# Kernel optimization log

Measured on AMD Instinct MI355X. Metric: run time of the kernel, lower is better.

Reference implementation:

```python
import jax, jax.numpy as jnp
import numpy as np
import math

D_MODEL = 1024
D_STATE = 16
D_CONV = 4
EXPAND = 2
D_INNER = EXPAND * D_MODEL
DT_RANK = math.ceil(D_MODEL / 16)
EPS = 1e-5


def setup_inputs() -> dict:
    key = jax.random.key(0)
    ks = jax.random.split(key, 8)
    B, L = 2, 1024
    s = 0.02
    return {
        "hidden_states": jax.random.normal(ks[0], (B, L, D_MODEL), jnp.float32),
        "norm_weight": jnp.ones((D_MODEL,), jnp.float32),
        "in_proj_w": (jax.random.normal(ks[1], (2 * D_INNER, D_MODEL), jnp.float32) * s),
        "conv_w": (jax.random.normal(ks[2], (D_INNER, D_CONV), jnp.float32) * s),
        "conv_b": jnp.zeros((D_INNER,), jnp.float32),
        "x_proj_w": (jax.random.normal(ks[3], (DT_RANK + 2 * D_STATE, D_INNER), jnp.float32) * s),
        "dt_proj_w": (jax.random.normal(ks[4], (D_INNER, DT_RANK), jnp.float32) * s),
        "dt_proj_b": jax.random.uniform(ks[5], (D_INNER,), jnp.float32, -4.0, -2.0),
        "A_log": jnp.log(jnp.broadcast_to(jnp.arange(1, D_STATE + 1, dtype=jnp.float32), (D_INNER, D_STATE))),
        "D": jnp.ones((D_INNER,), jnp.float32),
        "out_proj_w": (jax.random.normal(ks[6], (D_MODEL, D_INNER), jnp.float32) * s),
    }


def _rmsnorm(x, w):
    # Faithful to source: rms = ||x||_2 / sqrt(d); x / (rms + eps) * w
    norm = jnp.linalg.norm(x, axis=-1, keepdims=True)
    rms = norm * (1.0 / math.sqrt(x.shape[-1]))
    return w * (x / (rms + EPS))


def _mamba(h, in_proj_w, conv_w, conv_b, x_proj_w, dt_proj_w, dt_proj_b, A_log, D, out_proj_w):
    B, L, _ = h.shape
    xz = h @ in_proj_w.T                      # (B,L,2*D_INNER)
    x, z = jnp.split(xz, 2, axis=-1)          # each (B,L,D_INNER)

    # causal depthwise conv1d along L, kernel D_CONV
    xpad = jnp.pad(x, ((0, 0), (D_CONV - 1, 0), (0, 0)))
    xc = conv_b
    for k in range(D_CONV):                   # tiny fixed loop over kernel taps
        xc = xc + xpad[:, k:k + L, :] * conv_w[:, k]
    xc = jax.nn.silu(xc)                      # (B,L,D_INNER)

    x_dbl = xc @ x_proj_w.T                   # (B,L,DT_RANK+2N)
    dt, Bm, Cm = jnp.split(x_dbl, [DT_RANK, DT_RANK + D_STATE], axis=-1)
    dt = jax.nn.softplus(dt @ dt_proj_w.T + dt_proj_b)   # (B,L,D_INNER)

    A = -jnp.exp(A_log)                       # (D_INNER,N)
    deltaA = jnp.exp(dt[..., None] * A)                      # (B,L,D_INNER,N)
    deltaBu = (dt * xc)[..., None] * Bm[:, :, None, :]        # (B,L,D_INNER,N)

    def step(hst, inp):
        dA, dBu, Ct = inp
        hst = dA * hst + dBu                  # (B,D_INNER,N)
        y = jnp.einsum('bdn,bn->bd', hst, Ct)
        return hst, y

    h0 = jnp.zeros((B, D_INNER, D_STATE), xc.dtype)
    _, ys = jax.lax.scan(step, h0, (deltaA.swapaxes(0, 1), deltaBu.swapaxes(0, 1), Cm.swapaxes(0, 1)))
    y = ys.swapaxes(0, 1)                     # (B,L,D_INNER)
    y = y + D * xc
    y = y * jax.nn.silu(z)
    return y @ out_proj_w.T                   # (B,L,D_MODEL)


def reference(hidden_states, norm_weight, in_proj_w, conv_w, conv_b, x_proj_w,
              dt_proj_w, dt_proj_b, A_log, D, out_proj_w):
    residual = hidden_states
    h = _rmsnorm(residual, norm_weight)
    out = _mamba(h, in_proj_w, conv_w, conv_b, x_proj_w, dt_proj_w, dt_proj_b,
                 A_log, D, out_proj_w)
    return out, residual
```

## Files before the change

kernel.cpp:

```cpp
#include <hip/hip_runtime.h>

typedef __bf16 bf16x8 __attribute__((ext_vector_type(8)));
typedef float f32x4 __attribute__((ext_vector_type(4)));

__device__ __forceinline__ float b2f(ushort u) {
    union { unsigned int i; float f; } v;
    v.i = ((unsigned int)u) << 16;
    return v.f;
}
__device__ __forceinline__ ushort f2b(float f) {
    union { float f; unsigned int i; } v;
    v.f = f;
    unsigned int x = v.i;
    unsigned int r = (x + 0x7fffu + ((x >> 16) & 1u)) >> 16;
    return (ushort)r;
}
__device__ __forceinline__ float fexp2(float x) {
#if __has_builtin(__builtin_amdgcn_exp2f)
    return __builtin_amdgcn_exp2f(x);
#else
    return exp2f(x);
#endif
}
__device__ __forceinline__ unsigned int packb2(float ap, float h) {
    return ((unsigned int)f2b(h) << 16) | (unsigned int)f2b(ap);
}
__device__ __forceinline__ void gload16(const ushort* g, ushort* l) {
    __builtin_amdgcn_global_load_lds(
        (const __attribute__((address_space(1))) unsigned int*)g,
        (__attribute__((address_space(3))) unsigned int*)l, 16, 0, 0);
}
__device__ __forceinline__ bf16x8 ldsfrag(const ushort* s, int row, int cq) {
    int p = cq ^ (row & 7);
    return *(const bf16x8*)(s + row * 64 + p * 8);
}

#define D_MODEL 1024
#define D_INNER 2048
#define D_STATE 16
#define DT_RANK 64
#define NTOK    2048
#define LSEQ    1024
#define NCH     64
#define LC      16
#define KSL     16
#define LOG2E   1.44269504088896f

__global__ __launch_bounds__(256) void prep_kernel(
    const float* __restrict__ hs, const float* __restrict__ w,
    ushort* __restrict__ hout, float* __restrict__ resid,
    const float* __restrict__ inproj, const float* __restrict__ outproj,
    const float* __restrict__ xprojw, const float* __restrict__ dtw,
    ushort* __restrict__ wIn, ushort* __restrict__ wOut,
    ushort* __restrict__ xpw, ushort* __restrict__ dtwb,
    float* __restrict__ xdbl)
{
    int blk = blockIdx.x;
    int tid = threadIdx.x;
    if (blk < NTOK) {
        int t = blk;
        float4 r4 = *(const float4*)(hs + (size_t)t * D_MODEL + tid * 4);
        float s = r4.x * r4.x + r4.y * r4.y + r4.z * r4.z + r4.w * r4.w;
        #pragma unroll
        for (int off = 32; off >= 1; off >>= 1) s += __shfl_xor(s, off);
        __shared__ float red[4];
        int lane = tid & 63, wid = tid >> 6;
        if (lane == 0) red[wid] = s;
        __syncthreads();
        float tot = red[0] + red[1] + red[2] + red[3];
        float inv = 1.0f / (sqrtf(tot) * (1.0f / 32.0f) + 1e-5f);
        float4 w4 = *(const float4*)(w + tid * 4);
        ushort4 o;
        o.x = f2b(w4.x * r4.x * inv);
        o.y = f2b(w4.y * r4.y * inv);
        o.z = f2b(w4.z * r4.z * inv);
        o.w = f2b(w4.w * r4.w * inv);
        *(ushort4*)(hout + (size_t)t * D_MODEL + tid * 4) = o;
        *(float4*)(resid + (size_t)t * D_MODEL + tid * 4) = r4;
    } else if (blk < NTOK + 6464) {
        int i = (blk - NTOK) * 256 + tid;
        const float* src; ushort* dst; int off;
        if (i < 1048576)      { src = inproj;  dst = wIn;  off = i; }
        else if (i < 1572864) { src = outproj; dst = wOut; off = i - 1048576; }
        else if (i < 1622016) { src = xprojw;  dst = xpw;  off = i - 1572864; }
        else if (i < 1654784) { src = dtw;     dst = dtwb; off = i - 1622016; }
        else return;
        float4 v = *(const float4*)(src + (size_t)off * 4);
        ushort4 o;
        o.x = f2b(v.x); o.y = f2b(v.y); o.z = f2b(v.z); o.w = f2b(v.w);
        *(ushort4*)(dst + (size_t)off * 4) = o;
    } else {
        int i = (blk - NTOK - 6464) * 256 + tid;
        if (i < 49152)
            *(float4*)(xdbl + (size_t)i * 4) = (float4){0.f, 0.f, 0.f, 0.f};
    }
}

__global__ __launch_bounds__(512) void gemm_xz_kernel(
    const ushort* __restrict__ Ag, const ushort* __restrict__ Wg,
    const float* __restrict__ cw, const float* __restrict__ cb,
    ushort* __restrict__ xcb, ushort* __restrict__ xb,
    ushort* __restrict__ zq, int K)
{
    __shared__ __align__(16) ushort smem[128 * 128];
    __shared__ float cwl[128][4];
    __shared__ float cbl[128];
    ushort* sA = smem;
    ushort* sB = smem + 128 * 64;
    int tid = threadIdx.x;
    int bm = blockIdx.x, bn = blockIdx.y;
    int wid = tid >> 6, lane = tid & 63;
    int wm = (wid >> 1) * 32, wn = (wid & 1) * 64;
    int l16 = lane & 15, q = lane >> 4;
    int colbase = (bn & 15) * 128;

    if (bn < 16 && tid < 128) {
        cwl[tid][0] = cw[(size_t)(colbase + tid) * 4 + 0];
        cwl[tid][1] = cw[(size_t)(colbase + tid) * 4 + 1];
        cwl[tid][2] = cw[(size_t)(colbase + tid) * 4 + 2];
        cwl[tid][3] = cw[(size_t)(colbase + tid) * 4 + 3];
        cbl[tid] = cb[colbase + tid];
    }

    f32x4 acc[2][4];
    #pragma unroll
    for (int i = 0; i < 2; i++)
        #pragma unroll
        for (int j = 0; j < 4; j++)
            acc[i][j] = (f32x4){0.f, 0.f, 0.f, 0.f};

    const ushort* Abase = Ag + (size_t)bm * 128 * K;
    const ushort* Wbase = Wg + (size_t)bn * 128 * K;

    int segr = lane >> 3, segc = lane & 7;
    size_t goff[2]; int sseg[2];
    #pragma unroll
    for (int t = 0; t < 2; t++) {
        int s = wid * 2 + t;
        int r = s * 8 + segr;
        int gc = segc ^ (r & 7);
        sseg[t] = s * 512;
        goff[t] = (size_t)r * K + gc * 8;
    }

    for (int k0 = 0; k0 < K; k0 += 64) {
        __syncthreads();
        #pragma unroll
        for (int t = 0; t < 2; t++) {
            gload16(Abase + goff[t] + k0, sA + sseg[t]);
            gload16(Wbase + goff[t] + k0, sB + sseg[t]);
        }
        __syncthreads();
        #pragma unroll
        for (int ks = 0; ks < 2; ks++) {
            int cq = ks * 4 + q;
            bf16x8 af[2], bfr[4];
            #pragma unroll
            for (int i = 0; i < 2; i++)
                af[i] = ldsfrag(sA, wm + i * 16 + l16, cq);
            #pragma unroll
            for (int j = 0; j < 4; j++)
                bfr[j] = ldsfrag(sB, wn + j * 16 + l16, cq);
            #pragma unroll
            for (int i = 0; i < 2; i++)
                #pragma unroll
                for (int j = 0; j < 4; j++)
                    acc[i][j] = __builtin_amdgcn_mfma_f32_16x16x32_bf16(af[i], bfr[j], acc[i][j], 0, 0, 0);
        }
    }

    __syncthreads();
    #pragma unroll
    for (int i = 0; i < 2; i++)
        #pragma unroll
        for (int j = 0; j < 4; j++) {
            int col = wn + j * 16 + l16;
            int cchunk = col >> 3, cin = col & 7;
            #pragma unroll
            for (int r = 0; r < 4; r++) {
                int row = wm + i * 16 + q * 4 + r;
                smem[row * 128 + ((cchunk ^ (row & 7)) << 3) + cin] =
                    f2b(acc[i][j][r]);
            }
        }
    __syncthreads();
    size_t rowbase = (size_t)bm * 128;

    if (bn >= 16) {
        int cb2 = (bn - 16) * 128;
        #pragma unroll
        for (int it = 0; it < 4; it++) {
            int flat = it * 4096 + tid * 8;
            int row = flat >> 7, cchunk = (flat & 127) >> 3;
            *(uint4*)(zq + (rowbase + row) * D_INNER + cb2 + (cchunk << 3)) =
                *(const uint4*)(smem + row * 128 + ((cchunk ^ (row & 7)) << 3));
        }
        return;
    }

    if (tid < 96) {
        int rr = tid >> 4;
        int row = (rr < 3) ? rr : (125 + rr - 3);
        int chunk = tid & 15;
        *(uint4*)(xb + (size_t)(bm * 6 + rr) * D_INNER + colbase + chunk * 8) =
            *(const uint4*)(smem + row * 128 + ((chunk ^ (row & 7)) << 3));
    }

    for (int idx = tid; idx < 2000; idx += 512) {
        int row = (idx >> 4) + 3;
        int chunk = idx & 15;
        ushort tap[4][8];
        #pragma unroll
        for (int k = 0; k < 4; k++) {
            int rk = row - 3 + k;
            *(uint4*)tap[k] =
                *(const uint4*)(smem + rk * 128 + ((chunk ^ (rk & 7)) << 3));
        }
        ushort o[8];
        #pragma unroll
        for (int j = 0; j < 8; j++) {
            int cl = chunk * 8 + j;
            float acc2 = cbl[cl];
            #pragma unroll
            for (int k = 0; k < 4; k++)
                acc2 += b2f(tap[k][j]) * cwl[cl][k];
            o[j] = f2b(acc2 / (1.f + __expf(-acc2)));
        }
        *(uint4*)(xcb + (rowbase + row) * D_INNER + colbase + chunk * 8) =
            *(const uint4*)o;
    }
}

__global__ __launch_bounds__(256) void conv_fixup_kernel(
    const ushort* __restrict__ xb, const float* __restrict__ cw,
    const float* __restrict__ cb, ushort* __restrict__ xcb)
{
    int bm = blockIdx.x / 3;
    int r  = blockIdx.x % 3;
    int d0 = threadIdx.x * 8;

    ushort tap[4][8];
    bool has[4];
    #pragma unroll
    for (int k = 0; k < 4; k++) {
        int rt = r - 3 + k;
        if (rt < 0 && (bm & 7) == 0) {
            has[k] = false;
        } else {
            has[k] = true;
            int bmm, slot;
            if (rt < 0) { bmm = bm - 1; slot = rt + 6; }
            else        { bmm = bm;     slot = rt; }
            *(uint4*)tap[k] =
                *(const uint4*)(xb + (size_t)(bmm * 6 + slot) * D_INNER + d0);
        }
    }
    ushort o[8];
    #pragma unroll
    for (int j = 0; j < 8; j++) {
        float4 w4 = *(const float4*)(cw + (size_t)(d0 + j) * 4);
        float wk[4] = {w4.x, w4.y, w4.z, w4.w};
        float acc = cb[d0 + j];
        #pragma unroll
        for (int k = 0; k < 4; k++)
            if (has[k]) acc += b2f(tap[k][j]) * wk[k];
        o[j] = f2b(acc / (1.f + __expf(-acc)));
    }
    *(uint4*)(xcb + (size_t)(bm * 128 + r) * D_INNER + d0) = *(const uint4*)o;
}

__global__ __launch_bounds__(256) void gemm64_kernel(
    const ushort* __restrict__ Ag, const ushort* __restrict__ Wg,
    float* __restrict__ Cf, int M, int N, int K)
{
    __shared__ __align__(16) ushort smem[64 * 128];
    ushort* sA = smem;
    ushort* sB = smem + 64 * 64;
    float* fs = (float*)smem;
    int tid = threadIdx.x;
    int bm = blockIdx.x, bn = blockIdx.y;
    int wid = tid >> 6, lane = tid & 63;
    int wm = wid * 16;
    int l16 = lane & 15, q = lane >> 4;

    f32x4 acc[4];
    #pragma unroll
    for (int j = 0; j < 4; j++) acc[j] = (f32x4){0.f, 0.f, 0.f, 0.f};

    const ushort* Abase = Ag + (size_t)bm * 64 * K;
    const ushort* Wbase = Wg + (size_t)bn * 64 * K;

    int segr = lane >> 3, segc = lane & 7;
    size_t goff[2]; int sseg[2];
    #pragma unroll
    for (int t = 0; t < 2; t++) {
        int s = wid * 2 + t;
        int r = s * 8 + segr;
        int gc = segc ^ (r & 7);
        sseg[t] = s * 512;
        goff[t] = (size_t)r * K + gc * 8;
    }

    for (int k0 = 0; k0 < K; k0 += 64) {
        __syncthreads();
        #pragma unroll
        for (int t = 0; t < 2; t++) {
            gload16(Abase + goff[t] + k0, sA + sseg[t]);
            gload16(Wbase + goff[t] + k0, sB + sseg[t]);
        }
        __syncthreads();
        #pragma unroll
        for (int ks = 0; ks < 2; ks++) {
            int cq = ks * 4 + q;
            bf16x8 af = ldsfrag(sA, wm + l16, cq);
            bf16x8 bfr[4];
            #pragma unroll
            for (int j = 0; j < 4; j++)
                bfr[j] = ldsfrag(sB, j * 16 + l16, cq);
            #pragma unroll
            for (int j = 0; j < 4; j++)
                acc[j] = __builtin_amdgcn_mfma_f32_16x16x32_bf16(af, bfr[j], acc[j], 0, 0, 0);
        }
    }

    __syncthreads();
    #pragma unroll
    for (int j = 0; j < 4; j++)
        #pragma unroll
        for (int r = 0; r < 4; r++)
            fs[(wm + q * 4 + r) * 64 + j * 16 + l16] = acc[j][r];
    __syncthreads();
    #pragma unroll
    for (int it = 0; it < 4; it++) {
        int flat = it * 1024 + tid * 4;
        int row = flat >> 6, col = flat & 63;
        *(float4*)(Cf + (size_t)(bm * 64 + row) * N + bn * 64 + col) =
            *(const float4*)(fs + row * 64 + col);
    }
}

__global__ __launch_bounds__(256) void xproj_partial_kernel(
    const ushort* __restrict__ xcb, const ushort* __restrict__ wq,
    float* __restrict__ xdbl)
{
    __shared__ __align__(16) ushort sA[128 * 40];
    __shared__ __align__(16) ushort sB[96 * 40];
    int tid = threadIdx.x;
    int bm = blockIdx.x, sl = blockIdx.y;
    int wid = tid >> 6, lane = tid & 63;
    int wm = wid * 32;
    int l16 = lane & 15, q = lane >> 4;

    f32x4 acc[2][6];
    #pragma unroll
    for (int i = 0; i < 2; i++)
        #pragma unroll
        for (int j = 0; j < 6; j++)
            acc[i][j] = (f32x4){0.f, 0.f, 0.f, 0.f};

    const ushort* Abase = xcb + (size_t)bm * 128 * D_INNER;
    int kbase = sl * (D_INNER / KSL);

    for (int kk = 0; kk < D_INNER / KSL; kk += 32) {
        int k0 = kbase + kk;
        __syncthreads();
        #pragma unroll
        for (int i = tid; i < 512; i += 256) {
            int r = i >> 2, c = (i & 3) << 3;
            *(uint4*)(sA + r * 40 + c) = *(const uint4*)(Abase + (size_t)r * D_INNER + k0 + c);
        }
        for (int i = tid; i < 384; i += 256) {
            int r = i >> 2, c = (i & 3) << 3;
            *(uint4*)(sB + r * 40 + c) = *(const uint4*)(wq + (size_t)r * D_INNER + k0 + c);
        }
        __syncthreads();
        bf16x8 af[2], bfr[6];
        #pragma unroll
        for (int i = 0; i < 2; i++)
            af[i] = *(const bf16x8*)(sA + (wm + i * 16 + l16) * 40 + q * 8);
        #pragma unroll
        for (int j = 0; j < 6; j++)
            bfr[j] = *(const bf16x8*)(sB + (j * 16 + l16) * 40 + q * 8);
        #pragma unroll
        for (int i = 0; i < 2; i++)
            #pragma unroll
            for (int j = 0; j < 6; j++)
                acc[i][j] = __builtin_amdgcn_mfma_f32_16x16x32_bf16(af[i], bfr[j], acc[i][j], 0, 0, 0);
    }

    int row0 = bm * 128 + wm + q * 4;
    #pragma unroll
    for (int i = 0; i < 2; i++)
        #pragma unroll
        for (int j = 0; j < 6; j++)
            #pragma unroll
            for (int r = 0; r < 4; r++)
                atomicAdd(&xdbl[(size_t)(row0 + i * 16 + r) * 96 + j * 16 + l16],
                          acc[i][j][r]);
}

__global__ __launch_bounds__(256) void dt_gemm_kernel(
    const float* __restrict__ xdbl, const ushort* __restrict__ dtwq,
    const float* __restrict__ dtb, ushort* __restrict__ dtout)
{
    __shared__ __align__(16) ushort sA[64 * 72];
    __shared__ __align__(16) ushort sB[64 * 72];
    int tid = threadIdx.x;
    int bm = blockIdx.x, bn = blockIdx.y;
    int wid = tid >> 6, lane = tid & 63;
    int wm = wid * 16;
    int l16 = lane & 15, q = lane >> 4;

    const float* Abase = xdbl + (size_t)bm * 64 * 96;
    const ushort* Bbase = dtwq + (size_t)bn * 64 * DT_RANK;
    #pragma unroll
    for (int i = tid; i < 512; i += 256) {
        int r = i >> 3, c = (i & 7) << 3;
        float4 v0 = *(const float4*)(Abase + (size_t)r * 96 + c);
        float4 v1 = *(const float4*)(Abase + (size_t)r * 96 + c + 4);
        ushort o[8] = {f2b(v0.x), f2b(v0.y), f2b(v0.z), f2b(v0.w),
                       f2b(v1.x), f2b(v1.y), f2b(v1.z), f2b(v1.w)};
        *(uint4*)(sA + r * 72 + c) = *(const uint4*)o;
        *(uint4*)(sB + r * 72 + c) = *(const uint4*)(Bbase + (size_t)r * DT_RANK + c);
    }
    __syncthreads();

    f32x4 acc[4];
    #pragma unroll
    for (int j = 0; j < 4; j++) acc[j] = (f32x4){0.f, 0.f, 0.f, 0.f};

    #pragma unroll
    for (int ks = 0; ks < 2; ks++) {
        bf16x8 af = *(const bf16x8*)(sA + (wm + l16) * 72 + ks * 32 + q * 8);
        bf16x8 bfr[4];
        #pragma unroll
        for (int j = 0; j < 4; j++)
            bfr[j] = *(const bf16x8*)(sB + (j * 16 + l16) * 72 + ks * 32 + q * 8);
        #pragma unroll
        for (int j = 0; j < 4; j++)
            acc[j] = __builtin_amdgcn_mfma_f32_16x16x32_bf16(af, bfr[j], acc[j], 0, 0, 0);
    }

    __syncthreads();
    #pragma unroll
    for (int j = 0; j < 4; j++) {
        float bias = dtb[bn * 64 + j * 16 + l16];
        #pragma unroll
        for (int r = 0; r < 4; r++) {
            float s = acc[j][r] + bias;
            float sp = (s > 20.f) ? s : log1pf(__expf(s));
            sA[(wm + q * 4 + r) * 72 + j * 16 + l16] = f2b(sp);
        }
    }
    __syncthreads();
    int row0 = bm * 64, col0 = bn * 64;
    #pragma unroll
    for (int rep = 0; rep < 2; rep++) {
        int off = rep * 2048 + tid * 8;
        int row = off >> 6, col = off & 63;
        *(uint4*)(dtout + (size_t)(row0 + row) * D_INNER + col0 + col) =
            *(const uint4*)(sA + row * 72 + col);
    }
}

__global__ __launch_bounds__(256) void scan_partA_kernel(
    const ushort* __restrict__ dt, const ushort* __restrict__ xcq,
    const float* __restrict__ xdbl, const float* __restrict__ Alog,
    unsigned int* __restrict__ ch)
{
    __shared__ float sBC[LC][32];
    int bid = blockIdx.x;
    int g = bid & 7;
    int c = (bid >> 3) & (NCH - 1);
    int b = bid >> 9;
    int tid = threadIdx.x;
    int lane = tid & 63, wid = tid >> 6;
    int d = g * 256 + wid * 64 + lane;
    int l0 = c * LC;

    if (tid < LC * 8) {
        int r = tid >> 3, c4 = (tid & 7) * 4;
        *(float4*)&sBC[r][c4] =
            *(const float4*)(xdbl + ((size_t)(b * LSEQ + l0 + r)) * 96 + 64 + c4);
    }
    float A[16];
    #pragma unroll
    for (int k = 0; k < 4; k++)
        *(float4*)&A[k * 4] = *(const float4*)(Alog + d * D_STATE + k * 4);
    #pragma unroll
    for (int n = 0; n < 16; n++) A[n] = -__expf(A[n]) * LOG2E;
    __syncthreads();

    const ushort* dtp = dt  + ((size_t)(b * LSEQ + l0)) * D_INNER + d;
    const ushort* xcp = xcq + ((size_t)(b * LSEQ + l0)) * D_INNER + d;

    float h[16];
    #pragma unroll
    for (int n = 0; n < 16; n++) h[n] = 0.f;
    float S = 0.f;

    for (int l = 0; l < LC; l++) {
        float dtv = b2f(dtp[(size_t)l * D_INNER]);
        float xcv = b2f(xcp[(size_t)l * D_INNER]);
        float t = dtv * xcv;
        S += dtv;
        float Bv[16];
        #pragma unroll
        for (int k = 0; k < 4; k++)
            *(float4*)&Bv[k * 4] = *(const float4*)&sBC[l][k * 4];
        #pragma unroll
        for (int n = 0; n < 16; n++) {
            float a = fexp2(dtv * A[n]);
            h[n] = h[n] * a + t * Bv[n];
        }
    }

    unsigned int* outp = ch + (((size_t)(c * 2 + b)) << 15) + (d << 4);
    #pragma unroll
    for (int n = 0; n < 16; n += 4) {
        uint4 v;
        v.x = packb2(fexp2(A[n] * S),     h[n]);
        v.y = packb2(fexp2(A[n + 1] * S), h[n + 1]);
        v.z = packb2(fexp2(A[n + 2] * S), h[n + 2]);
        v.w = packb2(fexp2(A[n + 3] * S), h[n + 3]);
        *(uint4*)&outp[n] = v;
    }
}

__global__ __launch_bounds__(256) void scan_partB_kernel(
    const unsigned int* __restrict__ ch, ushort* __restrict__ hinit)
{
    int kk = blockIdx.x * 256 + threadIdx.x;
    int b = kk >> 15, dn = kk & 32767;
    float run = 0.f;
    #pragma unroll 8
    for (int c = 0; c < NCH; c++) {
        size_t off = (((size_t)(c * 2 + b)) << 15) + dn;
        unsigned int v = ch[off];
        hinit[off] = f2b(run);
        run = b2f((ushort)(v & 0xffffu)) * run + b2f((ushort)(v >> 16));
    }
}

__global__ __launch_bounds__(256) void scan_partC_kernel(
    const ushort* __restrict__ dt, const ushort* __restrict__ xcq,
    const float* __restrict__ xdbl, const ushort* __restrict__ zq,
    const float* __restrict__ Alog, const float* __restrict__ Dp,
    const ushort* __restrict__ hinit, ushort* __restrict__ yg)
{
    __shared__ float sBC[LC][32];
    int bid = blockIdx.x;
    int g = bid & 7;
    int c = (bid >> 3) & (NCH - 1);
    int b = bid >> 9;
    int tid = threadIdx.x;
    int lane = tid & 63, wid = tid >> 6;
    int d = g * 256 + wid * 64 + lane;
    int l0 = c * LC;

    if (tid < LC * 8) {
        int r = tid >> 3, c4 = (tid & 7) * 4;
        *(float4*)&sBC[r][c4] =
            *(const float4*)(xdbl + ((size_t)(b * LSEQ + l0 + r)) * 96 + 64 + c4);
    }
    float A[16];
    #pragma unroll
    for (int k = 0; k < 4; k++)
        *(float4*)&A[k * 4] = *(const float4*)(Alog + d * D_STATE + k * 4);
    #pragma unroll
    for (int n = 0; n < 16; n++) A[n] = -__expf(A[n]) * LOG2E;
    float Dd = Dp[d];

    const ushort* hp = hinit + (((size_t)(c * 2 + b)) << 15) + (d << 4);
    float h[16];
    #pragma unroll
    for (int n = 0; n < 16; n += 4) {
        ushort4 v = *(const ushort4*)(hp + n);
        h[n] = b2f(v.x); h[n + 1] = b2f(v.y);
        h[n + 2] = b2f(v.z); h[n + 3] = b2f(v.w);
    }
    __syncthreads();

    const ushort* dtp = dt  + ((size_t)(b * LSEQ + l0)) * D_INNER + d;
    const ushort* xcp = xcq + ((size_t)(b * LSEQ + l0)) * D_INNER + d;
    const ushort* zp  = zq  + ((size_t)(b * LSEQ + l0)) * D_INNER + d;
    ushort* yp = yg + ((size_t)(b * LSEQ + l0)) * D_INNER + d;

    for (int l = 0; l < LC; l++) {
        float dtv = b2f(dtp[(size_t)l * D_INNER]);
        float xcv = b2f(xcp[(size_t)l * D_INNER]);
        float zv  = b2f(zp[(size_t)l * D_INNER]);
        float t = dtv * xcv;
        float Bv[16], Cv[16];
        #pragma unroll
        for (int k = 0; k < 4; k++) {
            *(float4*)&Bv[k * 4] = *(const float4*)&sBC[l][k * 4];
            *(float4*)&Cv[k * 4] = *(const float4*)&sBC[l][16 + k * 4];
        }
        float p0 = 0.f, p1 = 0.f, p2 = 0.f, p3 = 0.f;
        #pragma unroll
        for (int n = 0; n < 16; n += 4) {
            float a0 = fexp2(dtv * A[n]);
            float a1 = fexp2(dtv * A[n + 1]);
            float a2 = fexp2(dtv * A[n + 2]);
            float a3 = fexp2(dtv * A[n + 3]);
            h[n]     = h[n] * a0 + t * Bv[n];
            h[n + 1] = h[n + 1] * a1 + t * Bv[n + 1];
            h[n + 2] = h[n + 2] * a2 + t * Bv[n + 2];
            h[n + 3] = h[n + 3] * a3 + t * Bv[n + 3];
            p0 += h[n] * Cv[n];
            p1 += h[n + 1] * Cv[n + 1];
            p2 += h[n + 2] * Cv[n + 2];
            p3 += h[n + 3] * Cv[n + 3];
        }
        float p = (p0 + p1) + (p2 + p3);
        float y = p + Dd * xcv;
        float sz = zv / (1.f + __expf(-zv));
        yp[(size_t)l * D_INNER] = f2b(y * sz);
    }
}

extern "C" void kernel_launch(void* const* d_in, const int* in_sizes, int n_in,
                              void* d_out, int out_size, void* d_ws, size_t ws_size,
                              hipStream_t stream)
{
    const float* hs      = (const float*)d_in[0];
    const float* norm_w  = (const float*)d_in[1];
    const float* inproj  = (const float*)d_in[2];
    const float* convw   = (const float*)d_in[3];
    const float* convb   = (const float*)d_in[4];
    const float* xprojw  = (const float*)d_in[5];
    const float* dtw     = (const float*)d_in[6];
    const float* dtb     = (const float*)d_in[7];
    const float* alog    = (const float*)d_in[8];
    const float* dvec    = (const float*)d_in[9];
    const float* outproj = (const float*)d_in[10];

    float* out_main  = (float*)d_out;
    float* out_resid = (float*)d_out + (size_t)NTOK * D_MODEL;

    char* ws = (char*)d_ws;
    ushort*       xb    = (ushort*)(ws);
    ushort*       zq    = (ushort*)(ws +  8388608);
    ushort*       dtq   = (ushort*)(ws + 16777216);
    ushort*       xcb   = (ushort*)(ws + 25165824);
    unsigned int* ch    = (unsigned int*)(ws + 33554432);
    ushort*       hinit = (ushort*)(ws + 50331648);
    float*        xdbl  = (float*) (ws + 67108864);
    ushort*       wIn   = (ushort*)(ws + 67895296);
    ushort*       wOut  = (ushort*)(ws + 76283904);
    ushort*       h_bf16= (ushort*)(ws + 80478208);
    ushort*       xpw_b = (ushort*)(ws + 84672512);
    ushort*       dtw_b = (ushort*)(ws + 85065728);
    ushort*       yg_bf16=(ushort*)(ws + 85327872);

    prep_kernel<<<NTOK + 6464 + 192, 256, 0, stream>>>(
        hs, norm_w, h_bf16, out_resid,
        inproj, outproj, xprojw, dtw, wIn, wOut, xpw_b, dtw_b, xdbl);

    gemm_xz_kernel<<<dim3(NTOK / 128, (2 * D_INNER) / 128), 512, 0, stream>>>(
        h_bf16, wIn, convw, convb, xcb, xb, zq, D_MODEL);

    conv_fixup_kernel<<<48, 256, 0, stream>>>(xb, convw, convb, xcb);

    xproj_partial_kernel<<<dim3(NTOK / 128, KSL), 256, 0, stream>>>(
        xcb, xpw_b, xdbl);

    dt_gemm_kernel<<<dim3(NTOK / 64, D_INNER / 64), 256, 0, stream>>>(
        xdbl, dtw_b, dtb, dtq);

    scan_partA_kernel<<<1024, 256, 0, stream>>>(dtq, xcb, xdbl, alog, ch);
    scan_partB_kernel<<<256, 256, 0, stream>>>(ch, hinit);
    scan_partC_kernel<<<1024, 256, 0, stream>>>(dtq, xcb, xdbl, zq,
                                                alog, dvec, hinit, yg_bf16);

    gemm64_kernel<<<dim3(NTOK / 64, D_MODEL / 64), 256, 0, stream>>>(
        yg_bf16, wOut, out_main, NTOK, D_MODEL, D_INNER);
}
```

Baseline: 227.9 us.

## Split-K out-projection with atomics and halve xproj tile rows for more blocks

```diff
diff --git a/kernel.cpp b/kernel.cpp
--- a/kernel.cpp
+++ b/kernel.cpp
@@ -53,7 +53,7 @@
     const float* __restrict__ xprojw, const float* __restrict__ dtw,
     ushort* __restrict__ wIn, ushort* __restrict__ wOut,
     ushort* __restrict__ xpw, ushort* __restrict__ dtwb,
-    float* __restrict__ xdbl)
+    float* __restrict__ xdbl, float* __restrict__ outz)
 {
     int blk = blockIdx.x;
     int tid = threadIdx.x;
@@ -89,10 +89,14 @@
         ushort4 o;
         o.x = f2b(v.x); o.y = f2b(v.y); o.z = f2b(v.z); o.w = f2b(v.w);
         *(ushort4*)(dst + (size_t)off * 4) = o;
-    } else {
+    } else if (blk < NTOK + 6464 + 192) {
         int i = (blk - NTOK - 6464) * 256 + tid;
         if (i < 49152)
             *(float4*)(xdbl + (size_t)i * 4) = (float4){0.f, 0.f, 0.f, 0.f};
+    } else {
+        int i = (blk - NTOK - 6464 - 192) * 256 + tid;
+        if (i < 524288)
+            *(float4*)(outz + (size_t)i * 4) = (float4){0.f, 0.f, 0.f, 0.f};
     }
 }
 
@@ -273,12 +277,10 @@
     const ushort* __restrict__ Ag, const ushort* __restrict__ Wg,
     float* __restrict__ Cf, int M, int N, int K)
 {
-    __shared__ __align__(16) ushort smem[64 * 128];
-    ushort* sA = smem;
-    ushort* sB = smem + 64 * 64;
-    float* fs = (float*)smem;
+    __shared__ __align__(16) ushort sA[64 * 64];
+    __shared__ __align__(16) ushort sB[64 * 64];
     int tid = threadIdx.x;
-    int bm = blockIdx.x, bn = blockIdx.y;
+    int bm = blockIdx.x, bn = blockIdx.y, bz = blockIdx.z;
     int wid = tid >> 6, lane = tid & 63;
     int wm = wid * 16;
     int l16 = lane & 15, q = lane >> 4;
@@ -301,7 +303,8 @@
         goff[t] = (size_t)r * K + gc * 8;
     }
 
-    for (int k0 = 0; k0 < K; k0 += 64) {
+    int kbeg = bz * (K / 2), kend = kbeg + K / 2;
+    for (int k0 = kbeg; k0 < kend; k0 += 64) {
         __syncthreads();
         #pragma unroll
         for (int t = 0; t < 2; t++) {
@@ -323,50 +326,40 @@
         }
     }
 
-    __syncthreads();
+    int row0 = bm * 64 + wm + q * 4;
+    int col0 = bn * 64 + l16;
     #pragma unroll
     for (int j = 0; j < 4; j++)
         #pragma unroll
         for (int r = 0; r < 4; r++)
-            fs[(wm + q * 4 + r) * 64 + j * 16 + l16] = acc[j][r];
-    __syncthreads();
-    #pragma unroll
-    for (int it = 0; it < 4; it++) {
-        int flat = it * 1024 + tid * 4;
-        int row = flat >> 6, col = flat & 63;
-        *(float4*)(Cf + (size_t)(bm * 64 + row) * N + bn * 64 + col) =
-            *(const float4*)(fs + row * 64 + col);
-    }
+            atomicAdd(&Cf[(size_t)(row0 + r) * N + col0 + j * 16], acc[j][r]);
 }
 
 __global__ __launch_bounds__(256) void xproj_partial_kernel(
     const ushort* __restrict__ xcb, const ushort* __restrict__ wq,
     float* __restrict__ xdbl)
 {
-    __shared__ __align__(16) ushort sA[128 * 40];
+    __shared__ __align__(16) ushort sA[64 * 40];
     __shared__ __align__(16) ushort sB[96 * 40];
     int tid = threadIdx.x;
     int bm = blockIdx.x, sl = blockIdx.y;
     int wid = tid >> 6, lane = tid & 63;
-    int wm = wid * 32;
+    int wm = wid * 16;
     int l16 = lane & 15, q = lane >> 4;
 
-    f32x4 acc[2][6];
-    #pragma unroll
-    for (int i = 0; i < 2; i++)
-        #pragma unroll
-        for (int j = 0; j < 6; j++)
-            acc[i][j] = (f32x4){0.f, 0.f, 0.f, 0.f};
-
-    const ushort* Abase = xcb + (size_t)bm * 128 * D_INNER;
+    f32x4 acc[6];
+    #pragma unroll
+    for (int j = 0; j < 6; j++)
+        acc[j] = (f32x4){0.f, 0.f, 0.f, 0.f};
+
+    const ushort* Abase = xcb + (size_t)bm * 64 * D_INNER;
     int kbase = sl * (D_INNER / KSL);
 
     for (int kk = 0; kk < D_INNER / KSL; kk += 32) {
         int k0 = kbase + kk;
         __syncthreads();
-        #pragma unroll
-        for (int i = tid; i < 512; i += 256) {
-            int r = i >> 2, c = (i & 3) << 3;
+        {
+            int r = tid >> 2, c = (tid & 3) << 3;
             *(uint4*)(sA + r * 40 + c) = *(const uint4*)(Abase + (size_t)r * D_INNER + k0 + c);
         }
         for (int i = tid; i < 384; i += 256) {
@@ -374,29 +367,22 @@
             *(uint4*)(sB + r * 40 + c) = *(const uint4*)(wq + (size_t)r * D_INNER + k0 + c);
         }
         __syncthreads();
-        bf16x8 af[2], bfr[6];
-        #pragma unroll
-        for (int i = 0; i < 2; i++)
-            af[i] = *(const bf16x8*)(sA + (wm + i * 16 + l16) * 40 + q * 8);
+        bf16x8 af = *(const bf16x8*)(sA + (wm + l16) * 40 + q * 8);
+        bf16x8 bfr[6];
         #pragma unroll
         for (int j = 0; j < 6; j++)
             bfr[j] = *(const bf16x8*)(sB + (j * 16 + l16) * 40 + q * 8);
         #pragma unroll
-        for (int i = 0; i < 2; i++)
-            #pragma unroll
-            for (int j = 0; j < 6; j++)
-                acc[i][j] = __builtin_amdgcn_mfma_f32_16x16x32_bf16(af[i], bfr[j], acc[i][j], 0, 0, 0);
-    }
-
-    int row0 = bm * 128 + wm + q * 4;
-    #pragma unroll
-    for (int i = 0; i < 2; i++)
-        #pragma unroll
         for (int j = 0; j < 6; j++)
-            #pragma unroll
-            for (int r = 0; r < 4; r++)
-                atomicAdd(&xdbl[(size_t)(row0 + i * 16 + r) * 96 + j * 16 + l16],
-                          acc[i][j][r]);
+            acc[j] = __builtin_amdgcn_mfma_f32_16x16x32_bf16(af, bfr[j], acc[j], 0, 0, 0);
+    }
+
+    int row0 = bm * 64 + wm + q * 4;
+    #pragma unroll
+    for (int j = 0; j < 6; j++)
+        #pragma unroll
+        for (int r = 0; r < 4; r++)
+            atomicAdd(&xdbl[(size_t)(row0 + r) * 96 + j * 16 + l16], acc[j][r]);
 }
 
 __global__ __launch_bounds__(256) void dt_gemm_kernel(
@@ -654,16 +640,16 @@
     ushort*       dtw_b = (ushort*)(ws + 85065728);
     ushort*       yg_bf16=(ushort*)(ws + 85327872);
 
-    prep_kernel<<<NTOK + 6464 + 192, 256, 0, stream>>>(
+    prep_kernel<<<NTOK + 6464 + 192 + 2048, 256, 0, stream>>>(
         hs, norm_w, h_bf16, out_resid,
-        inproj, outproj, xprojw, dtw, wIn, wOut, xpw_b, dtw_b, xdbl);
+        inproj, outproj, xprojw, dtw, wIn, wOut, xpw_b, dtw_b, xdbl, out_main);
 
     gemm_xz_kernel<<<dim3(NTOK / 128, (2 * D_INNER) / 128), 512, 0, stream>>>(
         h_bf16, wIn, convw, convb, xcb, xb, zq, D_MODEL);
 
     conv_fixup_kernel<<<48, 256, 0, stream>>>(xb, convw, convb, xcb);
 
-    xproj_partial_kernel<<<dim3(NTOK / 128, KSL), 256, 0, stream>>>(
+    xproj_partial_kernel<<<dim3(NTOK / 64, KSL), 256, 0, stream>>>(
         xcb, xpw_b, xdbl);
 
     dt_gemm_kernel<<<dim3(NTOK / 64, D_INNER / 64), 256, 0, stream>>>(
@@ -674,6 +660,6 @@
     scan_partC_kernel<<<1024, 256, 0, stream>>>(dtq, xcb, xdbl, zq,
                                                 alog, dvec, hinit, yg_bf16);
 
-    gemm64_kernel<<<dim3(NTOK / 64, D_MODEL / 64), 256, 0, stream>>>(
+    gemm64_kernel<<<dim3(NTOK / 64, D_MODEL / 64, 2), 256, 0, stream>>>(
         yg_bf16, wOut, out_main, NTOK, D_MODEL, D_INNER);
 }
```

New measurement: 228.0 us. Within noise of the previous version (+0.1%).
